# Kernel optimization log

Measured on AMD Instinct MI355X. Metric: run time of the kernel, lower is better.

Reference implementation:

```python
import jax, jax.numpy as jnp
import numpy as np

N_NODES = 50000
N_EDGES = 600000
N_GRAPHS = 512
LN_EPS = 1e-5


def setup_inputs() -> dict:
    key = jax.random.key(0)
    ks = jax.random.split(key, 18)
    s = 0.05
    return {
        "x": jax.random.normal(ks[0], (N_NODES, 29), jnp.float32),
        "xdims": jax.random.normal(ks[1], (N_NODES, 3), jnp.float32),
        "xsttype": jax.random.randint(ks[2], (N_NODES,), 0, 256),
        "edge_index": jax.random.randint(ks[3], (2, N_EDGES), 0, N_NODES),
        "batch": jnp.sort(jax.random.randint(ks[4], (N_NODES,), 0, N_GRAPHS)),
        "st_emb": jax.random.normal(ks[5], (256, 12), jnp.float32) * s,
        "Wl1": jax.random.normal(ks[6], (128, 44), jnp.float32) * s,
        "bl1": jnp.zeros((128,), jnp.float32),
        "Wr1": jax.random.normal(ks[7], (128, 44), jnp.float32) * s,
        "g1": jnp.ones((128,), jnp.float32),
        "beta1": jnp.zeros((128,), jnp.float32),
        "Wl2": jax.random.normal(ks[8], (128, 128), jnp.float32) * s,
        "bl2": jnp.zeros((128,), jnp.float32),
        "Wr2": jax.random.normal(ks[9], (128, 128), jnp.float32) * s,
        "g2": jnp.ones((128,), jnp.float32),
        "beta2": jnp.zeros((128,), jnp.float32),
        "Wlin": jax.random.normal(ks[10], (10, 256), jnp.float32) * s,
        "blin": jnp.zeros((10,), jnp.float32),
    }


def layernorm(h, g, b):
    mu = jnp.mean(h, axis=-1, keepdims=True)
    var = jnp.mean(jnp.square(h - mu), axis=-1, keepdims=True)
    return g * (h - mu) * jax.lax.rsqrt(var + LN_EPS) + b


def sage_conv(h, src, dst, Wl, bl, Wr):
    # PyG SAGEConv: lin_l(mean_j x_j) + lin_r(x_i); messages flow src -> dst.
    msg = h[src]                                            # [E, D]
    agg = jax.ops.segment_sum(msg, dst, num_segments=N_NODES)
    cnt = jax.ops.segment_sum(jnp.ones((msg.shape[0],), h.dtype), dst, num_segments=N_NODES)
    mean = agg / jnp.maximum(cnt, 1.0)[:, None]
    return mean @ Wl.T + bl + h @ Wr.T


def reference(x, xdims, xsttype, edge_index, batch, st_emb,
              Wl1, bl1, Wr1, g1, beta1,
              Wl2, bl2, Wr2, g2, beta2,
              Wlin, blin):
    src, dst = edge_index[0], edge_index[1]
    h = jnp.concatenate([x, xdims, st_emb[xsttype]], axis=1)   # [N, 44]
    # Layer 1
    h = jax.nn.relu(layernorm(sage_conv(h, src, dst, Wl1, bl1, Wr1), g1, beta1))
    # Layer 2
    h = jax.nn.relu(layernorm(sage_conv(h, src, dst, Wl2, bl2, Wr2), g2, beta2))
    # dropout inactive (inference)
    hs = jax.ops.segment_sum(h, batch, num_segments=N_GRAPHS)
    nc = jax.ops.segment_sum(jnp.ones((h.shape[0],), h.dtype), batch, num_segments=N_GRAPHS)
    hmean = hs / jnp.maximum(nc, 1.0)[:, None]
    hmax = jax.ops.segment_max(h, batch, num_segments=N_GRAPHS)
    pooled = jnp.concatenate([hmean, hmax], axis=1)            # [G, 256]
    return pooled @ Wlin.T + blin                              # [G, 10]
```

## Files before the change

### kernel.cpp

```cpp
#include <hip/hip_runtime.h>
#include <hip/hip_bf16.h>
#include <math.h>

#define N_NODES 50000
#define N_EDGES 600000
#define N_GRAPHS 512
#define LN_EPS 1e-5f
#define CAP 64
#define NPB 128
#define NBINS ((N_NODES + NPB - 1) / NPB)
#define BCAP 2048
#define BPAD 16
#define PREP_BLOCKS ((N_NODES * 8 + 255) / 256)

typedef short bf16x8 __attribute__((ext_vector_type(8)));
typedef float f32x4 __attribute__((ext_vector_type(4)));

__device__ __forceinline__ unsigned short f2bf(float f) {
    unsigned int x = __float_as_uint(f);
    return (unsigned short)((x + 0x7fffu + ((x >> 16) & 1u)) >> 16);
}
__device__ __forceinline__ float bflo(unsigned int u) { return __uint_as_float(u << 16); }
__device__ __forceinline__ float bfhi(unsigned int u) { return __uint_as_float(u & 0xffff0000u); }

__global__ __launch_bounds__(256) void prep_kernel(
    const float* __restrict__ x, const float* __restrict__ xdims,
    const int* __restrict__ stt, const float* __restrict__ st_emb,
    const float* __restrict__ Wl1, const float* __restrict__ Wr1,
    const float* __restrict__ Wl2, const float* __restrict__ Wr2,
    const int* __restrict__ batch,
    unsigned short* __restrict__ Xh1, unsigned short* __restrict__ Wc1,
    unsigned short* __restrict__ Wc2, int* __restrict__ binCnt,
    int* __restrict__ starts)
{
    int idx = blockIdx.x * 256 + threadIdx.x;

    if (idx < N_NODES * 8) {
        int n = idx >> 3;
        int c0 = (idx & 7) * 8;
        float vv[8];
        #pragma unroll
        for (int j = 0; j < 8; ++j) {
            int c = c0 + j;
            float v;
            if (c < 29)       v = x[n * 29 + c];
            else if (c < 32)  v = xdims[n * 3 + (c - 29)];
            else if (c < 44)  v = st_emb[stt[n] * 12 + (c - 32)];
            else              v = 0.f;
            vv[j] = v;
        }
        uint4 p;
        p.x = (unsigned int)f2bf(vv[0]) | ((unsigned int)f2bf(vv[1]) << 16);
        p.y = (unsigned int)f2bf(vv[2]) | ((unsigned int)f2bf(vv[3]) << 16);
        p.z = (unsigned int)f2bf(vv[4]) | ((unsigned int)f2bf(vv[5]) << 16);
        p.w = (unsigned int)f2bf(vv[6]) | ((unsigned int)f2bf(vv[7]) << 16);
        ((uint4*)Xh1)[idx] = p;
    }
    if (idx < 128 * 128) {
        int f = idx >> 7, k = idx & 127;
        float v;
        if (k < 44)        v = Wr1[f * 44 + k];
        else if (k < 64)   v = 0.f;
        else if (k < 108)  v = Wl1[f * 44 + (k - 64)];
        else               v = 0.f;
        Wc1[idx] = f2bf(v);
    }
    if (idx < 128 * 256) {
        int f = idx >> 8, k = idx & 255;
        float v = (k < 128) ? Wr2[f * 128 + k] : Wl2[f * 128 + (k - 128)];
        Wc2[idx] = f2bf(v);
    }
    if (idx < N_NODES) {
        int b = batch[idx];
        int pb = (idx == 0) ? -1 : batch[idx - 1];
        for (int g = pb + 1; g <= b; ++g) starts[g] = idx;
        if (idx == N_NODES - 1)
            for (int g = b + 1; g <= N_GRAPHS; ++g) starts[g] = N_NODES;
    }
    if (idx < NBINS * BPAD) binCnt[idx] = 0;
}

__global__ __launch_bounds__(1024) void bin_scatter_kernel(
    const int* __restrict__ esrc_in, const int* __restrict__ edst_in,
    int* __restrict__ binCnt, unsigned int* __restrict__ binBuf)
{
    __shared__ int cntL[NBINS];
    __shared__ int gbaseL[NBINS];
    const int tid = threadIdx.x;
    for (int i = tid; i < NBINS; i += 1024) cntL[i] = 0;
    __syncthreads();

    int e4 = (blockIdx.x * 1024 + tid) * 4;
    int4 d4, s4; int b0=0,b1=0,b2=0,b3=0, r0=0,r1=0,r2=0,r3=0;
    const bool valid = e4 < N_EDGES;
    if (valid) {
        d4 = *(const int4*)(edst_in + e4);
        s4 = *(const int4*)(esrc_in + e4);
        b0 = d4.x >> 7; b1 = d4.y >> 7; b2 = d4.z >> 7; b3 = d4.w >> 7;
        r0 = atomicAdd(&cntL[b0], 1);
        r1 = atomicAdd(&cntL[b1], 1);
        r2 = atomicAdd(&cntL[b2], 1);
        r3 = atomicAdd(&cntL[b3], 1);
    }
    __syncthreads();
    for (int i = tid; i < NBINS; i += 1024) {
        int c = cntL[i];
        gbaseL[i] = (c > 0) ? atomicAdd(&binCnt[i * BPAD], c) : 0;
    }
    __syncthreads();
    if (valid) {
        int p0 = gbaseL[b0] + r0, p1 = gbaseL[b1] + r1;
        int p2 = gbaseL[b2] + r2, p3 = gbaseL[b3] + r3;
        if (p0 < BCAP) binBuf[(size_t)b0 * BCAP + p0] = (((unsigned)d4.x & 127u) << 16) | (unsigned)s4.x;
        if (p1 < BCAP) binBuf[(size_t)b1 * BCAP + p1] = (((unsigned)d4.y & 127u) << 16) | (unsigned)s4.y;
        if (p2 < BCAP) binBuf[(size_t)b2 * BCAP + p2] = (((unsigned)d4.z & 127u) << 16) | (unsigned)s4.z;
        if (p3 < BCAP) binBuf[(size_t)b3 * BCAP + p3] = (((unsigned)d4.w & 127u) << 16) | (unsigned)s4.w;
    }
}

__global__ __launch_bounds__(256) void bin_adj_kernel(
    const int* __restrict__ binCnt, const unsigned int* __restrict__ binBuf,
    unsigned short* __restrict__ adj, int* __restrict__ cnt)
{
    __shared__ int cl[NPB];
    const int b = blockIdx.x;
    const int tid = threadIdx.x;
    if (tid < NPB) cl[tid] = 0;
    __syncthreads();
    int ec = binCnt[b * BPAD]; if (ec > BCAP) ec = BCAP;
    const unsigned int* buf = binBuf + (size_t)b * BCAP;
    for (int i = tid; i < ec; i += 256) {
        unsigned int p = buf[i];
        int dl = (int)(p >> 16);
        int slot = atomicAdd(&cl[dl], 1);
        if (slot < CAP)
            adj[((size_t)(b * NPB + dl)) * CAP + slot] = (unsigned short)(p & 0xFFFFu);
    }
    __syncthreads();
    if (tid < NPB) {
        int n = b * NPB + tid;
        if (n < N_NODES) cnt[n] = cl[tid];
    }
}

template <int DHALF>
__global__ __launch_bounds__(256) void agg_kernel(const int* __restrict__ cnt,
                                                  const unsigned short* __restrict__ adj,
                                                  const unsigned short* __restrict__ Xh,
                                                  unsigned short* __restrict__ M)
{
    constexpr int CH = DHALF / 8;
    constexpr int NG = 64 / CH;
    constexpr int NL = 16 / NG;
    int n = blockIdx.x * 4 + (threadIdx.x >> 6);
    if (n >= N_NODES) return;
    const int lane = threadIdx.x & 63;
    const int grp = lane / CH;
    const int sl  = lane % CH;
    int degT = cnt[n];
    int deg  = (degT < CAP) ? degT : CAP;
    int er = (int)adj[(size_t)n * CAP + lane];
    float a0=0.f,a1=0.f,a2=0.f,a3=0.f,a4=0.f,a5=0.f,a6=0.f,a7=0.f;
    const uint4* gbase = (const uint4*)Xh;
    const int c1 = deg - 1;
    for (int e = 0; e < deg; e += 16) {
        uint4 v[NL]; float mk[NL];
        #pragma unroll
        for (int j = 0; j < NL; ++j) {
            int ee = e + j * NG + grp;
            int s = __shfl(er, (ee < c1) ? ee : c1);
            v[j]  = gbase[(size_t)s * CH + sl];
            mk[j] = (ee < deg) ? 1.f : 0.f;
        }
        #pragma unroll
        for (int j = 0; j < NL; ++j) {
            a0 += mk[j] * bflo(v[j].x); a1 += mk[j] * bfhi(v[j].x);
            a2 += mk[j] * bflo(v[j].y); a3 += mk[j] * bfhi(v[j].y);
            a4 += mk[j] * bflo(v[j].z); a5 += mk[j] * bfhi(v[j].z);
            a6 += mk[j] * bflo(v[j].w); a7 += mk[j] * bfhi(v[j].w);
        }
    }
    #pragma unroll
    for (int m = CH; m <= 32; m <<= 1) {
        a0 += __shfl_xor(a0, m); a1 += __shfl_xor(a1, m);
        a2 += __shfl_xor(a2, m); a3 += __shfl_xor(a3, m);
        a4 += __shfl_xor(a4, m); a5 += __shfl_xor(a5, m);
        a6 += __shfl_xor(a6, m); a7 += __shfl_xor(a7, m);
    }
    if (grp == 0) {
        float inv = (degT > 0) ? 1.f / (float)degT : 0.f;
        uint4 p;
        p.x = (unsigned int)f2bf(a0 * inv) | ((unsigned int)f2bf(a1 * inv) << 16);
        p.y = (unsigned int)f2bf(a2 * inv) | ((unsigned int)f2bf(a3 * inv) << 16);
        p.z = (unsigned int)f2bf(a4 * inv) | ((unsigned int)f2bf(a5 * inv) << 16);
        p.w = (unsigned int)f2bf(a6 * inv) | ((unsigned int)f2bf(a7 * inv) << 16);
        ((uint4*)M)[(size_t)n * CH + sl] = p;
    }
}

template <int KPAD>
__global__ __launch_bounds__(256) void mfma_layer_kernel(
    const unsigned short* __restrict__ Xh, const unsigned short* __restrict__ M,
    const unsigned short* __restrict__ W,
    const float* __restrict__ bl, const float* __restrict__ g,
    const float* __restrict__ beta,
    unsigned short* __restrict__ Out)
{
    constexpr int DHALF = KPAD / 2;
    const int lane = threadIdx.x & 63;
    const int wv   = threadIdx.x >> 6;
    const int l15  = lane & 15;
    const int l4   = lane >> 4;
    const int row0 = blockIdx.x * 128 + wv * 32;

    int rA0 = row0 + l15;       if (rA0 > N_NODES - 1) rA0 = N_NODES - 1;
    int rA1 = row0 + 16 + l15;  if (rA1 > N_NODES - 1) rA1 = N_NODES - 1;

    f32x4 acc[2][8];
    #pragma unroll
    for (int m = 0; m < 2; ++m)
        #pragma unroll
        for (int n = 0; n < 8; ++n) acc[m][n] = (f32x4){0.f, 0.f, 0.f, 0.f};

    const int kb = l4 * 8;
    #pragma unroll
    for (int ks = 0; ks < KPAD / 32; ++ks) {
        const int k = ks * 32 + kb;
        bf16x8 a0, a1;
        if (ks < DHALF / 32) {
            a0 = *(const bf16x8*)(Xh + (size_t)rA0 * DHALF + k);
            a1 = *(const bf16x8*)(Xh + (size_t)rA1 * DHALF + k);
        } else {
            a0 = *(const bf16x8*)(M + (size_t)rA0 * DHALF + (k - DHALF));
            a1 = *(const bf16x8*)(M + (size_t)rA1 * DHALF + (k - DHALF));
        }
        #pragma unroll
        for (int ni = 0; ni < 8; ++ni) {
            bf16x8 b = *(const bf16x8*)(W + (size_t)(ni * 16 + l15) * KPAD + k);
            acc[0][ni] = __builtin_amdgcn_mfma_f32_16x16x32_bf16(a0, b, acc[0][ni], 0, 0, 0);
            acc[1][ni] = __builtin_amdgcn_mfma_f32_16x16x32_bf16(a1, b, acc[1][ni], 0, 0, 0);
        }
    }

    float blv[8], gv[8], bev[8];
    #pragma unroll
    for (int ni = 0; ni < 8; ++ni) {
        int f = ni * 16 + l15;
        blv[ni] = bl[f]; gv[ni] = g[f]; bev[ni] = beta[f];
    }

    #pragma unroll
    for (int mi = 0; mi < 2; ++mi) {
        #pragma unroll
        for (int r = 0; r < 4; ++r) {
            float v[8];
            float s1 = 0.f, s2 = 0.f;
            #pragma unroll
            for (int ni = 0; ni < 8; ++ni) {
                float t = acc[mi][ni][r] + blv[ni];
                v[ni] = t; s1 += t; s2 += t * t;
            }
            #pragma unroll
            for (int m = 8; m >= 1; m >>= 1) {
                s1 += __shfl_xor(s1, m);
                s2 += __shfl_xor(s2, m);
            }
            float mu   = s1 * (1.f / 128.f);
            float var  = s2 * (1.f / 128.f) - mu * mu;
            float rstd = rsqrtf(var + LN_EPS);
            int node = row0 + mi * 16 + l4 * 4 + r;
            if (node < N_NODES) {
                #pragma unroll
                for (int ni = 0; ni < 8; ++ni) {
                    float o = gv[ni] * (v[ni] - mu) * rstd + bev[ni];
                    o = fmaxf(o, 0.f);
                    Out[(size_t)node * 128 + ni * 16 + l15] = f2bf(o);
                }
            }
        }
    }
}

__global__ __launch_bounds__(256) void poolhead_kernel(const unsigned short* __restrict__ h2,
                                                       const int* __restrict__ starts,
                                                       const float* __restrict__ Wlin,
                                                       const float* __restrict__ blin,
                                                       float* __restrict__ out)
{
    const int g  = blockIdx.x;
    const int j2 = threadIdx.x & 63;
    const int h  = threadIdx.x >> 6;
    const int s0 = starts[g], s1 = starts[g + 1];
    float sa = 0.f, sb = 0.f, ma = -INFINITY, mb = -INFINITY;
    const unsigned int* base = (const unsigned int*)h2;
    int n = s0 + h;
    for (; n + 4 < s1; n += 8) {
        unsigned int u0 = base[(size_t)n * 64 + j2];
        unsigned int u1 = base[(size_t)(n + 4) * 64 + j2];
        float l0 = bflo(u0), h0 = bfhi(u0);
        float l1 = bflo(u1), h1 = bfhi(u1);
        sa += l0 + l1; sb += h0 + h1;
        ma = fmaxf(ma, fmaxf(l0, l1));
        mb = fmaxf(mb, fmaxf(h0, h1));
    }
    if (n < s1) {
        unsigned int u = base[(size_t)n * 64 + j2];
        float lo = bflo(u), hi = bfhi(u);
        sa += lo; sb += hi;
        ma = fmaxf(ma, lo); mb = fmaxf(mb, hi);
    }
    __shared__ float red[4][4][64];
    __shared__ float pooled[256];
    red[h][0][j2] = sa; red[h][1][j2] = sb; red[h][2][j2] = ma; red[h][3][j2] = mb;
    __syncthreads();
    if (h == 0) {
        #pragma unroll
        for (int o = 1; o < 4; ++o) {
            sa += red[o][0][j2]; sb += red[o][1][j2];
            ma = fmaxf(ma, red[o][2][j2]); mb = fmaxf(mb, red[o][3][j2]);
        }
        int c = s1 - s0;
        float inv = (c > 0) ? 1.f / (float)c : 0.f;
        pooled[2 * j2]           = sa * inv;
        pooled[2 * j2 + 1]       = sb * inv;
        pooled[128 + 2 * j2]     = (c > 0) ? ma : 0.f;
        pooled[128 + 2 * j2 + 1] = (c > 0) ? mb : 0.f;
    }
    __syncthreads();
    if (threadIdx.x < 10) {
        const float* w = Wlin + threadIdx.x * 256;
        float acc = blin[threadIdx.x];
        for (int k = 0; k < 256; ++k) acc += pooled[k] * w[k];
        out[g * 10 + threadIdx.x] = acc;
    }
}

extern "C" void kernel_launch(void* const* d_in, const int* in_sizes, int n_in,
                              void* d_out, int out_size, void* d_ws, size_t ws_size,
                              hipStream_t stream)
{
    const float* x      = (const float*)d_in[0];
    const float* xdims  = (const float*)d_in[1];
    const int*   stt    = (const int*)d_in[2];
    const int*   eidx   = (const int*)d_in[3];
    const int*   batch  = (const int*)d_in[4];
    const float* st_emb = (const float*)d_in[5];
    const float* Wl1 = (const float*)d_in[6];
    const float* bl1 = (const float*)d_in[7];
    const float* Wr1 = (const float*)d_in[8];
    const float* g1  = (const float*)d_in[9];
    const float* be1 = (const float*)d_in[10];
    const float* Wl2 = (const float*)d_in[11];
    const float* bl2 = (const float*)d_in[12];
    const float* Wr2 = (const float*)d_in[13];
    const float* g2  = (const float*)d_in[14];
    const float* be2 = (const float*)d_in[15];
    const float* Wlin = (const float*)d_in[16];
    const float* blin = (const float*)d_in[17];
    float* out = (float*)d_out;

    const int* esrc_in = eidx;
    const int* edst_in = eidx + N_EDGES;

    char* ws = (char*)d_ws;
    size_t o = 0;
    auto carve = [&](size_t bytes) { void* p = ws + o; o = (o + bytes + 255) & ~(size_t)255; return p; };
    unsigned short* Xh1  = (unsigned short*)carve((size_t)N_NODES * 64 * 2);
    unsigned short* M1   = (unsigned short*)carve((size_t)N_NODES * 64 * 2);
    unsigned short* Xh2  = (unsigned short*)carve((size_t)N_NODES * 128 * 2);
    unsigned short* M2   = (unsigned short*)carve((size_t)N_NODES * 128 * 2);
    unsigned short* h2bf = (unsigned short*)carve((size_t)N_NODES * 128 * 2);
    unsigned short* Wc1  = (unsigned short*)carve((size_t)128 * 128 * 2);
    unsigned short* Wc2  = (unsigned short*)carve((size_t)128 * 256 * 2);
    int*            cnt  = (int*)carve((size_t)N_NODES * 4);
    int*          binCnt = (int*)carve((size_t)NBINS * BPAD * 4);
    unsigned int* binBuf = (unsigned int*)carve((size_t)NBINS * BCAP * 4);
    unsigned short* adj  = (unsigned short*)carve((size_t)(NBINS * NPB) * CAP * 2);
    int*          starts = (int*)carve((size_t)(N_GRAPHS + 1) * 4);
    (void)ws_size;

    prep_kernel<<<PREP_BLOCKS, 256, 0, stream>>>(
        x, xdims, stt, st_emb, Wl1, Wr1, Wl2, Wr2, batch,
        Xh1, Wc1, Wc2, binCnt, starts);

    bin_scatter_kernel<<<(N_EDGES / 4 + 1023) / 1024, 1024, 0, stream>>>(
        esrc_in, edst_in, binCnt, binBuf);

    bin_adj_kernel<<<NBINS, 256, 0, stream>>>(binCnt, binBuf, adj, cnt);

    agg_kernel<64><<<(N_NODES + 3) / 4, 256, 0, stream>>>(cnt, adj, Xh1, M1);
    mfma_layer_kernel<128><<<(N_NODES + 127) / 128, 256, 0, stream>>>(
        Xh1, M1, Wc1, bl1, g1, be1, Xh2);

    agg_kernel<128><<<(N_NODES + 3) / 4, 256, 0, stream>>>(cnt, adj, Xh2, M2);
    mfma_layer_kernel<256><<<(N_NODES + 127) / 128, 256, 0, stream>>>(
        Xh2, M2, Wc2, bl2, g2, be2, h2bf);

    poolhead_kernel<<<N_GRAPHS, 256, 0, stream>>>(h2bf, starts, Wlin, blin, out);
}
```

Before: 116.1 us.

## Pack multiple nodes per wavefront in neighbor aggregation kernels

The aggregation kernel now processes NPW nodes per 64-lane wavefront (4 for layer 1, 2 for layer 2) instead of one. Each node's adjacency entries are loaded as packed 32-bit pairs and unpacked after a shuffle. Edges beyond the shuffled window fall back to direct adjacency loads, and the cross-group reduction shrinks to a single xor step. The aim is to cut idle lanes and wasted reduction work, since the average degree is about 12 while the old loop stepped 16 edges at a time across a full wave. The launch grid assumes N_NODES divides evenly and the bounds check is gone, which holds for 50000.

```diff
diff --git a/kernel.cpp b/kernel.cpp
--- a/kernel.cpp
+++ b/kernel.cpp
@@ -143,32 +143,39 @@
     }
 }
 
-template <int DHALF>
+template <int DHALF, int NPW>
 __global__ __launch_bounds__(256) void agg_kernel(const int* __restrict__ cnt,
                                                   const unsigned short* __restrict__ adj,
                                                   const unsigned short* __restrict__ Xh,
                                                   unsigned short* __restrict__ M)
 {
-    constexpr int CH = DHALF / 8;
-    constexpr int NG = 64 / CH;
-    constexpr int NL = 16 / NG;
-    int n = blockIdx.x * 4 + (threadIdx.x >> 6);
-    if (n >= N_NODES) return;
+    constexpr int CH  = DHALF / 8;
+    constexpr int LPN = 64 / NPW;
+    constexpr int NG  = LPN / CH;
+    constexpr int NL  = 16 / NG;
     const int lane = threadIdx.x & 63;
-    const int grp = lane / CH;
-    const int sl  = lane % CH;
+    const int wv   = threadIdx.x >> 6;
+    const int ln   = lane % LPN;
+    const int nbl  = lane - ln;
+    const int grp  = ln / CH;
+    const int sl   = ln % CH;
+    const int n = (blockIdx.x * 4 + wv) * NPW + (lane / LPN);
+
     int degT = cnt[n];
     int deg  = (degT < CAP) ? degT : CAP;
-    int er = (int)adj[(size_t)n * CAP + lane];
+    unsigned int er32 = ((const unsigned int*)adj)[(size_t)n * (CAP / 2) + ln];
     float a0=0.f,a1=0.f,a2=0.f,a3=0.f,a4=0.f,a5=0.f,a6=0.f,a7=0.f;
     const uint4* gbase = (const uint4*)Xh;
     const int c1 = deg - 1;
-    for (int e = 0; e < deg; e += 16) {
+    const int lim1 = (2 * LPN >= CAP) ? deg : ((deg < 2 * LPN) ? deg : 2 * LPN);
+    for (int e = 0; e < lim1; e += 16) {
         uint4 v[NL]; float mk[NL];
         #pragma unroll
         for (int j = 0; j < NL; ++j) {
             int ee = e + j * NG + grp;
-            int s = __shfl(er, (ee < c1) ? ee : c1);
+            int eec = (ee < c1) ? ee : c1;
+            unsigned int u = __shfl(er32, nbl + (eec >> 1));
+            int s = (eec & 1) ? (int)(u >> 16) : (int)(u & 0xFFFFu);
             v[j]  = gbase[(size_t)s * CH + sl];
             mk[j] = (ee < deg) ? 1.f : 0.f;
         }
@@ -180,13 +187,31 @@
             a6 += mk[j] * bflo(v[j].w); a7 += mk[j] * bfhi(v[j].w);
         }
     }
-    #pragma unroll
-    for (int m = CH; m <= 32; m <<= 1) {
-        a0 += __shfl_xor(a0, m); a1 += __shfl_xor(a1, m);
-        a2 += __shfl_xor(a2, m); a3 += __shfl_xor(a3, m);
-        a4 += __shfl_xor(a4, m); a5 += __shfl_xor(a5, m);
-        a6 += __shfl_xor(a6, m); a7 += __shfl_xor(a7, m);
-    }
+    if (2 * LPN < CAP) {
+        for (int e = 2 * LPN; e < deg; e += 16) {
+            uint4 v[NL]; float mk[NL];
+            #pragma unroll
+            for (int j = 0; j < NL; ++j) {
+                int ee = e + j * NG + grp;
+                int eec = (ee < c1) ? ee : c1;
+                int s = (int)adj[(size_t)n * CAP + eec];
+                v[j]  = gbase[(size_t)s * CH + sl];
+                mk[j] = (ee < deg) ? 1.f : 0.f;
+            }
+            #pragma unroll
+            for (int j = 0; j < NL; ++j) {
+                a0 += mk[j] * bflo(v[j].x); a1 += mk[j] * bfhi(v[j].x);
+                a2 += mk[j] * bflo(v[j].y); a3 += mk[j] * bfhi(v[j].y);
+                a4 += mk[j] * bflo(v[j].z); a5 += mk[j] * bfhi(v[j].z);
+                a6 += mk[j] * bflo(v[j].w); a7 += mk[j] * bfhi(v[j].w);
+            }
+        }
+    }
+    a0 += __shfl_xor(a0, CH); a1 += __shfl_xor(a1, CH);
+    a2 += __shfl_xor(a2, CH); a3 += __shfl_xor(a3, CH);
+    a4 += __shfl_xor(a4, CH); a5 += __shfl_xor(a5, CH);
+    a6 += __shfl_xor(a6, CH); a7 += __shfl_xor(a7, CH);
+
     if (grp == 0) {
         float inv = (degT > 0) ? 1.f / (float)degT : 0.f;
         uint4 p;
@@ -388,11 +413,11 @@
 
     bin_adj_kernel<<<NBINS, 256, 0, stream>>>(binCnt, binBuf, adj, cnt);
 
-    agg_kernel<64><<<(N_NODES + 3) / 4, 256, 0, stream>>>(cnt, adj, Xh1, M1);
+    agg_kernel<64, 4><<<N_NODES / 16, 256, 0, stream>>>(cnt, adj, Xh1, M1);
     mfma_layer_kernel<128><<<(N_NODES + 127) / 128, 256, 0, stream>>>(
         Xh1, M1, Wc1, bl1, g1, be1, Xh2);
 
-    agg_kernel<128><<<(N_NODES + 3) / 4, 256, 0, stream>>>(cnt, adj, Xh2, M2);
+    agg_kernel<128, 2><<<N_NODES / 8, 256, 0, stream>>>(cnt, adj, Xh2, M2);
     mfma_layer_kernel<256><<<(N_NODES + 127) / 128, 256, 0, stream>>>(
         Xh2, M2, Wc2, bl2, g2, be2, h2bf);
 
```

Measured after the change: 112.5 us. 1.03x faster.
